# Kernel optimization log

Hardware: AMD Instinct MI355X
Metric: run time of the kernel (lower is better)

Reference implementation:

```python
import math
import jax, jax.numpy as jnp
import numpy as np

B, N, F, FE = 16, 24, 128, 128   # crystals, atoms/crystal, atom feat, edge feat
NUM_Z = 100                       # num_atomic_numbers
GAUSS_STOP, BASIS_W = 6.0, 1.0
RADIUS_RATE = 1.0
N_CONV, N_FC, FC_F = 3, 4, 128
REP = 1                           # PBC replication per axis (27 images); exact for our cells
ZDIM = 2 * F + FE


def setup_inputs() -> dict:
    key = jax.random.key(0)
    ks = jax.random.split(key, 12)
    # cubic cells with side length in [8, 10) Angstrom -> rep per axis is exactly 1
    L = 8.0 + 2.0 * jax.random.uniform(ks[0], (B,))
    cell = L[:, None, None] * jnp.eye(3, dtype=jnp.float32)          # [B,3,3]
    frac = jax.random.uniform(ks[1], (B, N, 3))
    pos = jnp.einsum('bnd,bde->bne', frac, cell).reshape(B * N, 3)   # [B*N,3]
    atomic_numbers = jax.random.randint(ks[2], (B * N,), 1, NUM_Z + 1)
    batch = jnp.repeat(jnp.arange(B), N)
    emb = jax.random.normal(ks[3], (NUM_Z, F)) * 0.1                 # embedding table
    s = 1.0 / math.sqrt(ZDIM)
    conv_Wf = jax.random.normal(ks[4], (N_CONV, ZDIM, F)) * s
    conv_bf = jnp.zeros((N_CONV, F))
    conv_Ws = jax.random.normal(ks[5], (N_CONV, ZDIM, F)) * s
    conv_bs = jnp.zeros((N_CONV, F))
    sf = 1.0 / math.sqrt(FC_F)
    fc_W = jax.random.normal(ks[6], (N_FC - 1, FC_F, FC_F)) * sf
    fc_b = jnp.zeros((N_FC - 1, FC_F))
    W_out = jax.random.normal(ks[7], (FC_F, 1)) * sf
    b_out = jnp.zeros((1,))
    return {'pos': pos, 'cell': cell, 'emb': emb,
            'conv_Wf': conv_Wf, 'conv_bf': conv_bf,
            'conv_Ws': conv_Ws, 'conv_bs': conv_bs,
            'fc_W': fc_W, 'fc_b': fc_b, 'W_out': W_out, 'b_out': b_out,
            'atomic_numbers': atomic_numbers, 'batch': batch}


def _spectral_normalize(W, iters=5, eps=1e-12):
    # power iteration; sigma differentiable through W only (u,v detached) as in torch
    u = jnp.ones((W.shape[1],), W.dtype)
    u = u / jnp.linalg.norm(u)
    for _ in range(iters):
        v = W @ u
        v = v / (jnp.linalg.norm(v) + eps)
        u = W.T @ v
        u = u / (jnp.linalg.norm(u) + eps)
    u = jax.lax.stop_gradient(u)
    v = jax.lax.stop_gradient(v)
    sigma = v @ (W @ u)
    return W / sigma


def _forward(pos, cell, emb, conv_Wf, conv_bf, conv_Ws, conv_bs,
             fc_W, fc_b, W_out, b_out, atomic_numbers):
    # ---- graph construction (PBC all-pairs, fixed 27 images, masked) ----
    r = jnp.arange(-REP, REP + 1, dtype=cell.dtype)
    grid = jnp.stack(jnp.meshgrid(r, r, r, indexing='ij'), -1).reshape(-1, 3)  # [27,3]
    pbc = jnp.einsum('cd,bde->bce', grid, cell)                                # [B,27,3]
    posb = pos.reshape(B, N, 3)
    # disp[b,i,j,c] = pos_i - (pos_j + offset_c)
    disp = posb[:, :, None, None, :] - (posb[:, None, :, None, :] + pbc[:, None, None, :, :])
    dsqr = jnp.sum(disp * disp, -1)                                            # [B,N,N,27]
    cross = jnp.cross(cell[:, 1], cell[:, 2])
    vol = jnp.sum(cell[:, 0] * cross, -1)
    radius = RADIUS_RATE * (jnp.abs(vol) / N) ** (1.0 / 3.0)                   # [B]
    rb = radius[:, None, None, None]
    mask = (dsqr <= rb * rb) & (dsqr > 1e-4)
    dist = jnp.sqrt(jnp.maximum(dsqr, 1e-12))
    mf = mask.astype(pos.dtype)
    edge_w = (jnp.cos(dist * math.pi / rb) + 1.0) * mf                         # [B,N,N,27]
    # GaussianSmearing
    goff = jnp.linspace(0.0, GAUSS_STOP, FE)
    coeff = -0.5 / (BASIS_W * (goff[1] - goff[0])) ** 2
    edge_attr = jnp.exp(coeff * (dist[..., None] - goff) ** 2)                 # [B,N,N,27,FE]

    # ---- node features ----
    feat = jnp.tanh(emb[atomic_numbers - 1]).reshape(B, N, F)

    # ---- continuous graph convs (CGCNN-style gated conv, edge_weight scaled) ----
    for l in range(N_CONV):
        Wf, Ws = conv_Wf[l], conv_Ws[l]
        gi = feat @ Wf[:F]; gj = feat @ Wf[F:2 * F]
        ge = jnp.einsum('bijce,ef->bijcf', edge_attr, Wf[2 * F:])
        g = jax.nn.sigmoid(gi[:, :, None, None, :] + gj[:, None, :, None, :] + ge + conv_bf[l])
        si = feat @ Ws[:F]; sj = feat @ Ws[F:2 * F]
        se = jnp.einsum('bijce,ef->bijcf', edge_attr, Ws[2 * F:])
        sc = jax.nn.softplus(si[:, :, None, None, :] + sj[:, None, :, None, :] + se + conv_bs[l])
        msg = g * sc * edge_w[..., None]                                       # [B,N,N,27,F]
        feat = jax.nn.softplus(feat + msg.sum((2, 3)))                         # aggregate at i

    # ---- global mean pool + spectral-norm MLP head ----
    h = feat.mean(1)                                                           # [B,F]
    for l in range(N_FC - 1):
        h = jax.nn.softplus(h @ _spectral_normalize(fc_W[l]) + fc_b[l])
    return h @ W_out + b_out                                                   # [B,1]


def reference(pos, cell, emb, conv_Wf, conv_bf, conv_Ws, conv_bs,
              fc_W, fc_b, W_out, b_out, atomic_numbers, batch):
    return _forward(pos, cell, emb, conv_Wf, conv_bf, conv_Ws, conv_bs,
                    fc_W, fc_b, W_out, b_out, atomic_numbers)
```

## Files before the change

kernel.cpp:

```cpp
#include <hip/hip_runtime.h>
#include <math.h>

#define NB 16
#define NN 24
#define NA 384
#define FF 128
#define CC 27
#define MAXNBR 32

__device__ int   g_cnt[NA];
__device__ float g_sigma[4];
__device__ int   g_nj[NA*MAXNBR];
__device__ float g_nd[NA*MAXNBR];
__device__ float g_nw[NA*MAXNBR];
__device__ float g_featA[NA*FF];
__device__ float g_featB[NA*FF];
__device__ float g_projA[NA*4*FF];
__device__ float g_projB[NA*4*FF];
__device__ float g_feat [NA*FF];
__device__ int   g_arrF[NB];

__device__ __forceinline__ float softplusf(float x){ return fmaxf(x,0.f) + log1pf(expf(-fabsf(x))); }
__device__ __forceinline__ float sigmoidf(float x){ return 1.f/(1.f+expf(-x)); }
__device__ __forceinline__ void st_agent(float* p, float v){
  __hip_atomic_store(p, v, __ATOMIC_RELAXED, __HIP_MEMORY_SCOPE_AGENT);
}
__device__ __forceinline__ float ld_agent(const float* p){
  return __hip_atomic_load(p, __ATOMIC_RELAXED, __HIP_MEMORY_SCOPE_AGENT);
}

__device__ __forceinline__ void band_dot(float dist, const float* __restrict__ Wf2,
                                         const float* __restrict__ Ws2, int f,
                                         float& ge, float& se)
{
  const float step  = 6.0f/127.0f;
  const float coeff = -0.5f/(step*step);
  int kmin = (int)ceilf(dist/step - 9.0f);
  kmin = kmin < 0 ? 0 : (kmin > 108 ? 108 : kmin);
  float g = 0.f, s = 0.f;
  #pragma unroll
  for (int t = 0; t < 20; t++) {
    int k = kmin + t;
    float dd = dist - step*(float)k;
    float a  = expf(coeff*dd*dd);
    g += a * Wf2[k*FF+f];
    s += a * Ws2[k*FF+f];
  }
  ge = g; se = s;
}

__global__ void __launch_bounds__(512)
k_prep(const float* __restrict__ pos, const float* __restrict__ cell,
       const float* __restrict__ emb, const float* __restrict__ fc_W,
       const float* __restrict__ conv_Wf, const float* __restrict__ conv_Ws,
       const int* __restrict__ z)
{
  const int bid = blockIdx.x, tid = threadIdx.x;
  const int q = tid >> 7, f = tid & 127;

  if (bid < 3) {
    __shared__ float s_w[FF*129];
    __shared__ float s_u[FF], s_v[FF], s_red[FF];
    __shared__ float s_part[4][FF];
    const float* W = fc_W + bid*FF*FF;
    for (int idx = tid; idx < FF*FF; idx += 512)
      s_w[(idx >> 7)*129 + (idx & 127)] = W[idx];
    if (tid < FF) s_u[tid] = 0.08838834764831845f;
    __syncthreads();
    for (int it = 0; it < 5; it++) {
      { float p = 0.f;
        #pragma unroll
        for (int k = q*32; k < q*32+32; k++) p += s_w[f*129+k]*s_u[k];
        s_part[q][f] = p; }
      __syncthreads();
      if (tid < FF) { float s = s_part[0][f]+s_part[1][f]+s_part[2][f]+s_part[3][f];
                      s_v[f] = s; s_red[f] = s*s; }
      __syncthreads();
      for (int st=64; st>0; st>>=1){ if (tid<st) s_red[tid]+=s_red[tid+st]; __syncthreads(); }
      float nv = sqrtf(s_red[0]) + 1e-12f;
      __syncthreads();
      if (tid < FF) s_v[f] /= nv;
      __syncthreads();
      { float p = 0.f;
        #pragma unroll
        for (int r = q*32; r < q*32+32; r++) p += s_w[r*129+f]*s_v[r];
        s_part[q][f] = p; }
      __syncthreads();
      if (tid < FF) { float s = s_part[0][f]+s_part[1][f]+s_part[2][f]+s_part[3][f];
                      s_u[f] = s; s_red[f] = s*s; }
      __syncthreads();
      for (int st=64; st>0; st>>=1){ if (tid<st) s_red[tid]+=s_red[tid+st]; __syncthreads(); }
      float nu = sqrtf(s_red[0]) + 1e-12f;
      __syncthreads();
      if (tid < FF) s_u[f] /= nu;
      __syncthreads();
    }
    { float p = 0.f;
      #pragma unroll
      for (int k = q*32; k < q*32+32; k++) p += s_w[f*129+k]*s_u[k];
      s_part[q][f] = p; }
    __syncthreads();
    if (tid < FF) s_red[f] = s_v[f]*(s_part[0][f]+s_part[1][f]+s_part[2][f]+s_part[3][f]);
    __syncthreads();
    for (int st=64; st>0; st>>=1){ if (tid<st) s_red[tid]+=s_red[tid+st]; __syncthreads(); }
    if (tid == 0) g_sigma[bid] = s_red[0];
  } else {
    const int i = bid - 3;
    const int b = i / NN;
    __shared__ float ft[FF];
    __shared__ float s_cell[9];
    __shared__ float s_rb;
    __shared__ int   s_cnt;
    if (tid < FF) {
      int zi = z[i]; if (zi < 1) zi = 1; if (zi > 100) zi = 100;
      float v = tanhf(emb[(zi-1)*FF+tid]);
      ft[tid] = v;
      g_featA[i*FF+tid] = v;
    }
    if (tid >= 256 && tid < 265) s_cell[tid-256] = cell[b*9 + tid - 256];
    if (tid == 500) s_cnt = 0;
    __syncthreads();
    if (tid == 0) {
      const float* c = s_cell;
      float cx = c[4]*c[8] - c[5]*c[7];
      float cy = c[5]*c[6] - c[3]*c[8];
      float cz = c[3]*c[7] - c[4]*c[6];
      float vol = c[0]*cx + c[1]*cy + c[2]*cz;
      s_rb = cbrtf(fabsf(vol)/(float)NN);
    }
    __syncthreads();
    const float rb = s_rb, rb2 = rb*rb;
    const float pix = pos[i*3+0], piy = pos[i*3+1], piz = pos[i*3+2];
    const float PI = 3.14159265358979323846f;
    for (int cand = tid; cand < NN*CC; cand += 512) {
      int j = cand / CC, c = cand - j*CC;
      float gx = (float)(c/9) - 1.0f;
      float gy = (float)((c/3)%3) - 1.0f;
      float gz = (float)(c%3) - 1.0f;
      float ox = gx*s_cell[0] + gy*s_cell[3] + gz*s_cell[6];
      float oy = gx*s_cell[1] + gy*s_cell[4] + gz*s_cell[7];
      float oz = gx*s_cell[2] + gy*s_cell[5] + gz*s_cell[8];
      int jg = b*NN + j;
      float dx = pix - (pos[jg*3+0] + ox);
      float dy = piy - (pos[jg*3+1] + oy);
      float dz = piz - (pos[jg*3+2] + oz);
      float d2 = dx*dx + dy*dy + dz*dz;
      if (d2 <= rb2 && d2 > 1e-4f) {
        float dist = sqrtf(fmaxf(d2, 1e-12f));
        float w = cosf(dist*PI/rb) + 1.0f;
        int slot = atomicAdd(&s_cnt, 1);
        if (slot < MAXNBR) {
          g_nj[i*MAXNBR+slot] = jg;
          g_nd[i*MAXNBR+slot] = dist;
          g_nw[i*MAXNBR+slot] = w;
        }
      }
    }
    __syncthreads();
    if (tid == 0) g_cnt[i] = (s_cnt > MAXNBR) ? MAXNBR : s_cnt;
    const float* W = (q==0) ? conv_Wf
                   : (q==1) ? (conv_Wf + FF*FF)
                   : (q==2) ? conv_Ws
                   :          (conv_Ws + FF*FF);
    float s = 0.f;
    #pragma unroll 16
    for (int k=0;k<FF;k++) s += ft[k]*W[k*FF+f];
    g_projA[(i*4+q)*FF+f] = s;
  }
}

template<int LAYER>
__global__ void __launch_bounds__(512)
k_edge(const float* __restrict__ conv_Wf, const float* __restrict__ conv_bf,
       const float* __restrict__ conv_Ws, const float* __restrict__ conv_bs)
{
  const int i = blockIdx.x, tid = threadIdx.x;
  const int q = tid >> 7, f = tid & 127;
  const float* projSrc = (LAYER==0) ? g_projA : g_projB;
  float*       projDst = (LAYER==0) ? g_projB : g_projA;
  const float* fin  = (LAYER==0) ? g_featA : g_featB;
  float*       fout = (LAYER==0) ? g_featB : g_featA;
  const float* Wf2 = conv_Wf + LAYER*3*FF*FF + 2*FF*FF;
  const float* Ws2 = conv_Ws + LAYER*3*FF*FF + 2*FF*FF;

  const float gi  = projSrc[(i*4+0)*FF+f];
  const float si  = projSrc[(i*4+2)*FF+f];
  const float bff = conv_bf[LAYER*FF+f];
  const float bsf = conv_bs[LAYER*FF+f];
  const int n = g_cnt[i];

  float msg = 0.f;
  for (int e = q; e < n; e += 4) {
    const int   jg   = g_nj[i*MAXNBR+e];
    const float dist = g_nd[i*MAXNBR+e];
    const float w    = g_nw[i*MAXNBR+e];
    const float gj   = projSrc[(jg*4+1)*FF+f];
    const float sj   = projSrc[(jg*4+3)*FF+f];
    float ge, se;
    band_dot(dist, Wf2, Ws2, f, ge, se);
    msg += sigmoidf(gi + gj + ge + bff) * softplusf(si + sj + se + bsf) * w;
  }

  __shared__ float sm[4][FF];
  __shared__ float fnew[FF];
  sm[q][f] = msg;
  __syncthreads();
  if (tid < FF) {
    float v = softplusf(fin[i*FF+f] + sm[0][f] + sm[1][f] + sm[2][f] + sm[3][f]);
    fnew[f] = v;
    fout[i*FF+f] = v;
  }
  __syncthreads();
  const float* WfN = conv_Wf + (LAYER+1)*3*FF*FF;
  const float* WsN = conv_Ws + (LAYER+1)*3*FF*FF;
  const float* W = (q==0) ? WfN : (q==1) ? (WfN + FF*FF) : (q==2) ? WsN : (WsN + FF*FF);
  float s = 0.f;
  #pragma unroll 16
  for (int k=0;k<FF;k++) s += fnew[k]*W[k*FF+f];
  projDst[(i*4+q)*FF+f] = s;
}

__global__ void __launch_bounds__(512)
k_edge2f(const float* __restrict__ conv_Wf, const float* __restrict__ conv_bf,
         const float* __restrict__ conv_Ws, const float* __restrict__ conv_bs,
         const float* __restrict__ fc_W,  const float* __restrict__ fc_b,
         const float* __restrict__ W_out, const float* __restrict__ b_out,
         float* __restrict__ out)
{
  const int i = blockIdx.x, tid = threadIdx.x;
  const int q = tid >> 7, f = tid & 127;
  const int b = i / NN;
  const float* Wf2 = conv_Wf + 2*3*FF*FF + 2*FF*FF;
  const float* Ws2 = conv_Ws + 2*3*FF*FF + 2*FF*FF;

  const float gi  = g_projA[(i*4+0)*FF+f];
  const float si  = g_projA[(i*4+2)*FF+f];
  const float bff = conv_bf[2*FF+f];
  const float bsf = conv_bs[2*FF+f];
  const int n = g_cnt[i];

  float msg = 0.f;
  for (int e = q; e < n; e += 4) {
    const int   jg   = g_nj[i*MAXNBR+e];
    const float dist = g_nd[i*MAXNBR+e];
    const float w    = g_nw[i*MAXNBR+e];
    const float gj   = g_projA[(jg*4+1)*FF+f];
    const float sj   = g_projA[(jg*4+3)*FF+f];
    float ge, se;
    band_dot(dist, Wf2, Ws2, f, ge, se);
    msg += sigmoidf(gi + gj + ge + bff) * softplusf(si + sj + se + bsf) * w;
  }

  __shared__ float sm[4][FF];
  __shared__ int   s_old;
  sm[q][f] = msg;
  __syncthreads();
  if (tid < FF) {
    float v = softplusf(g_featA[i*FF+f] + sm[0][f] + sm[1][f] + sm[2][f] + sm[3][f]);
    st_agent(&g_feat[i*FF+f], v);
  }
  asm volatile("s_waitcnt vmcnt(0)" ::: "memory");
  __syncthreads();
  if (tid == 0)
    s_old = __hip_atomic_fetch_add(&g_arrF[b], 1, __ATOMIC_ACQ_REL,
                                   __HIP_MEMORY_SCOPE_AGENT);
  __syncthreads();
  if (s_old != NN-1) return;

  __shared__ float s_hh[FF], s_tmp[FF], s_part[4][FF], s_red[FF];
  if (tid < FF) {
    float s0 = 0.f;
    for (int a = 0; a < NN; a++) s0 += ld_agent(&g_feat[(b*NN+a)*FF+tid]);
    s_hh[tid] = s0/(float)NN;
  }
  __syncthreads();
  for (int l = 0; l < 3; l++) {
    { float p = 0.f;
      #pragma unroll
      for (int k = q*32; k < q*32+32; k++) p += s_hh[k]*fc_W[l*FF*FF + k*FF + f];
      s_part[q][f] = p; }
    __syncthreads();
    if (tid < FF) {
      float s = s_part[0][tid]+s_part[1][tid]+s_part[2][tid]+s_part[3][tid];
      s_tmp[tid] = softplusf(s/g_sigma[l] + fc_b[l*FF+tid]);
    }
    __syncthreads();
    if (tid < FF) s_hh[tid] = s_tmp[tid];
    __syncthreads();
  }
  if (tid < FF) s_red[tid] = s_hh[tid]*W_out[tid];
  __syncthreads();
  if (tid < 64) {
    float t = s_red[tid] + s_red[tid+64];
    #pragma unroll
    for (int off = 32; off > 0; off >>= 1) t += __shfl_xor(t, off);
    if (tid == 0) {
      out[b] = t + b_out[0];
      __hip_atomic_store(&g_arrF[b], 0, __ATOMIC_RELAXED,
                         __HIP_MEMORY_SCOPE_AGENT);
    }
  }
}

extern "C" void kernel_launch(void* const* d_in, const int* in_sizes, int n_in,
                              void* d_out, int out_size, void* d_ws, size_t ws_size,
                              hipStream_t stream) {
  const float* pos     = (const float*)d_in[0];
  const float* cell    = (const float*)d_in[1];
  const float* emb     = (const float*)d_in[2];
  const float* conv_Wf = (const float*)d_in[3];
  const float* conv_bf = (const float*)d_in[4];
  const float* conv_Ws = (const float*)d_in[5];
  const float* conv_bs = (const float*)d_in[6];
  const float* fc_W    = (const float*)d_in[7];
  const float* fc_b    = (const float*)d_in[8];
  const float* W_out   = (const float*)d_in[9];
  const float* b_out   = (const float*)d_in[10];
  const int*   z       = (const int*)d_in[11];

  k_prep   <<<NA+3, 512, 0, stream>>>(pos, cell, emb, fc_W, conv_Wf, conv_Ws, z);
  k_edge<0><<<NA,   512, 0, stream>>>(conv_Wf, conv_bf, conv_Ws, conv_bs);
  k_edge<1><<<NA,   512, 0, stream>>>(conv_Wf, conv_bf, conv_Ws, conv_bs);
  k_edge2f <<<NA,   512, 0, stream>>>(conv_Wf, conv_bf, conv_Ws, conv_bs,
                                      fc_W, fc_b, W_out, b_out, (float*)d_out);
}
```

Measured before the change: 138.5 us.

## Fuse all stages into one persistent kernel with per-crystal spin barriers

Replaces the four kernel launches with a single fused kernel. Each atom block keeps its neighbor list, features and projections in shared memory, and blocks of the same crystal synchronize through global atomic counters instead of kernel boundaries. This removes launch gaps and global round-trips for neighbor lists and features, and the spectral-norm blocks now read weights straight from global memory rather than staging them in LDS. It relies on all 387 blocks being co-resident, otherwise the spin-waits can deadlock or hit the guard and compute wrong results.

```diff
diff --git a/kernel.cpp b/kernel.cpp
--- a/kernel.cpp
+++ b/kernel.cpp
@@ -8,17 +8,13 @@
 #define CC 27
 #define MAXNBR 32
 
-__device__ int   g_cnt[NA];
 __device__ float g_sigma[4];
-__device__ int   g_nj[NA*MAXNBR];
-__device__ float g_nd[NA*MAXNBR];
-__device__ float g_nw[NA*MAXNBR];
-__device__ float g_featA[NA*FF];
-__device__ float g_featB[NA*FF];
 __device__ float g_projA[NA*4*FF];
 __device__ float g_projB[NA*4*FF];
 __device__ float g_feat [NA*FF];
-__device__ int   g_arrF[NB];
+__device__ int   g_cnt4 [4*NB];
+__device__ int   g_sigdone;
+__device__ int   g_batchdone;
 
 __device__ __forceinline__ float softplusf(float x){ return fmaxf(x,0.f) + log1pf(expf(-fabsf(x))); }
 __device__ __forceinline__ float sigmoidf(float x){ return 1.f/(1.f+expf(-x)); }
@@ -49,86 +45,165 @@
   ge = g; se = s;
 }
 
-__global__ void __launch_bounds__(512)
-k_prep(const float* __restrict__ pos, const float* __restrict__ cell,
-       const float* __restrict__ emb, const float* __restrict__ fc_W,
-       const float* __restrict__ conv_Wf, const float* __restrict__ conv_Ws,
-       const int* __restrict__ z)
-{
-  const int bid = blockIdx.x, tid = threadIdx.x;
+__device__ __forceinline__ float gemv_q(const float* __restrict__ Wf,
+                                        const float* __restrict__ Ws,
+                                        const float* s_ft, int q, int f)
+{
+  const float* W = (q==0) ? Wf : (q==1) ? (Wf + FF*FF) : (q==2) ? Ws : (Ws + FF*FF);
+  float s = 0.f;
+  #pragma unroll 16
+  for (int k = 0; k < FF; k++) s += s_ft[k]*W[k*FF+f];
+  return s;
+}
+
+__device__ __forceinline__ void publish(int* ctr)
+{
+  asm volatile("s_waitcnt vmcnt(0)" ::: "memory");
+  __syncthreads();
+  if (threadIdx.x == 0)
+    __hip_atomic_fetch_add(ctr, 1, __ATOMIC_RELEASE, __HIP_MEMORY_SCOPE_AGENT);
+}
+
+__device__ __forceinline__ void wait_ge(int* ctr, int target)
+{
+  if (threadIdx.x == 0) {
+    int guard = 0;
+    while (__hip_atomic_load(ctr, __ATOMIC_ACQUIRE, __HIP_MEMORY_SCOPE_AGENT) < target) {
+      __builtin_amdgcn_s_sleep(2);
+      if (++guard > (1<<20)) break;
+    }
+  }
+  __syncthreads();
+}
+
+__device__ __forceinline__ void edge_layer(int l, int q, int f, int n, int i,
+       const float* __restrict__ projSrc,
+       const float* __restrict__ conv_Wf, const float* __restrict__ conv_bf,
+       const float* __restrict__ conv_Ws, const float* __restrict__ conv_bs,
+       const int* s_nj, const float* s_nd, const float* s_nw,
+       float (*s_p)[FF], float (*sm)[FF], float* s_ft)
+{
+  const float* Wf2 = conv_Wf + l*3*FF*FF + 2*FF*FF;
+  const float* Ws2 = conv_Ws + l*3*FF*FF + 2*FF*FF;
+  const float gi  = s_p[0][f];
+  const float si  = s_p[2][f];
+  const float bff = conv_bf[l*FF+f];
+  const float bsf = conv_bs[l*FF+f];
+  float msg = 0.f;
+  for (int e = q; e < n; e += 4) {
+    const int   jg   = s_nj[e];
+    const float dist = s_nd[e];
+    const float w    = s_nw[e];
+    const float gj   = ld_agent(&projSrc[(jg*4+1)*FF+f]);
+    const float sj   = ld_agent(&projSrc[(jg*4+3)*FF+f]);
+    float ge, se;
+    band_dot(dist, Wf2, Ws2, f, ge, se);
+    msg += sigmoidf(gi + gj + ge + bff) * softplusf(si + sj + se + bsf) * w;
+  }
+  sm[q][f] = msg;
+  __syncthreads();
+  if (threadIdx.x < FF) {
+    float v = softplusf(s_ft[f] + sm[0][f] + sm[1][f] + sm[2][f] + sm[3][f]);
+    s_ft[f] = v;
+  }
+  __syncthreads();
+}
+
+__global__ void __launch_bounds__(512, 4)
+k_fused(const float* __restrict__ pos, const float* __restrict__ cell,
+        const float* __restrict__ emb,
+        const float* __restrict__ conv_Wf, const float* __restrict__ conv_bf,
+        const float* __restrict__ conv_Ws, const float* __restrict__ conv_bs,
+        const float* __restrict__ fc_W,  const float* __restrict__ fc_b,
+        const float* __restrict__ W_out, const float* __restrict__ b_out,
+        const int* __restrict__ z, float* __restrict__ out)
+{
+  const int tid = threadIdx.x;
   const int q = tid >> 7, f = tid & 127;
 
-  if (bid < 3) {
-    __shared__ float s_w[FF*129];
-    __shared__ float s_u[FF], s_v[FF], s_red[FF];
-    __shared__ float s_part[4][FF];
-    const float* W = fc_W + bid*FF*FF;
-    for (int idx = tid; idx < FF*FF; idx += 512)
-      s_w[(idx >> 7)*129 + (idx & 127)] = W[idx];
+  if (blockIdx.x < 3) {
+    const int m = blockIdx.x;
+    const float* W = fc_W + m*FF*FF;
+    __shared__ float s_u[FF], s_v[FF], s_red2[FF];
+    __shared__ float s_part2[4][FF];
     if (tid < FF) s_u[tid] = 0.08838834764831845f;
     __syncthreads();
     for (int it = 0; it < 5; it++) {
       { float p = 0.f;
         #pragma unroll
-        for (int k = q*32; k < q*32+32; k++) p += s_w[f*129+k]*s_u[k];
-        s_part[q][f] = p; }
-      __syncthreads();
-      if (tid < FF) { float s = s_part[0][f]+s_part[1][f]+s_part[2][f]+s_part[3][f];
-                      s_v[f] = s; s_red[f] = s*s; }
-      __syncthreads();
-      for (int st=64; st>0; st>>=1){ if (tid<st) s_red[tid]+=s_red[tid+st]; __syncthreads(); }
-      float nv = sqrtf(s_red[0]) + 1e-12f;
+        for (int k = q*32; k < q*32+32; k++) p += W[f*FF+k]*s_u[k];
+        s_part2[q][f] = p; }
+      __syncthreads();
+      if (tid < FF) { float s = s_part2[0][f]+s_part2[1][f]+s_part2[2][f]+s_part2[3][f];
+                      s_v[f] = s; s_red2[f] = s*s; }
+      __syncthreads();
+      for (int st=64; st>0; st>>=1){ if (tid<st) s_red2[tid]+=s_red2[tid+st]; __syncthreads(); }
+      float nv = sqrtf(s_red2[0]) + 1e-12f;
       __syncthreads();
       if (tid < FF) s_v[f] /= nv;
       __syncthreads();
       { float p = 0.f;
         #pragma unroll
-        for (int r = q*32; r < q*32+32; r++) p += s_w[r*129+f]*s_v[r];
-        s_part[q][f] = p; }
-      __syncthreads();
-      if (tid < FF) { float s = s_part[0][f]+s_part[1][f]+s_part[2][f]+s_part[3][f];
-                      s_u[f] = s; s_red[f] = s*s; }
-      __syncthreads();
-      for (int st=64; st>0; st>>=1){ if (tid<st) s_red[tid]+=s_red[tid+st]; __syncthreads(); }
-      float nu = sqrtf(s_red[0]) + 1e-12f;
+        for (int r = q*32; r < q*32+32; r++) p += W[r*FF+f]*s_v[r];
+        s_part2[q][f] = p; }
+      __syncthreads();
+      if (tid < FF) { float s = s_part2[0][f]+s_part2[1][f]+s_part2[2][f]+s_part2[3][f];
+                      s_u[f] = s; s_red2[f] = s*s; }
+      __syncthreads();
+      for (int st=64; st>0; st>>=1){ if (tid<st) s_red2[tid]+=s_red2[tid+st]; __syncthreads(); }
+      float nu = sqrtf(s_red2[0]) + 1e-12f;
       __syncthreads();
       if (tid < FF) s_u[f] /= nu;
       __syncthreads();
     }
     { float p = 0.f;
       #pragma unroll
-      for (int k = q*32; k < q*32+32; k++) p += s_w[f*129+k]*s_u[k];
-      s_part[q][f] = p; }
-    __syncthreads();
-    if (tid < FF) s_red[f] = s_v[f]*(s_part[0][f]+s_part[1][f]+s_part[2][f]+s_part[3][f]);
-    __syncthreads();
-    for (int st=64; st>0; st>>=1){ if (tid<st) s_red[tid]+=s_red[tid+st]; __syncthreads(); }
-    if (tid == 0) g_sigma[bid] = s_red[0];
-  } else {
-    const int i = bid - 3;
-    const int b = i / NN;
-    __shared__ float ft[FF];
-    __shared__ float s_cell[9];
-    __shared__ float s_rb;
-    __shared__ int   s_cnt;
-    if (tid < FF) {
-      int zi = z[i]; if (zi < 1) zi = 1; if (zi > 100) zi = 100;
-      float v = tanhf(emb[(zi-1)*FF+tid]);
-      ft[tid] = v;
-      g_featA[i*FF+tid] = v;
-    }
-    if (tid >= 256 && tid < 265) s_cell[tid-256] = cell[b*9 + tid - 256];
-    if (tid == 500) s_cnt = 0;
-    __syncthreads();
+      for (int k = q*32; k < q*32+32; k++) p += W[f*FF+k]*s_u[k];
+      s_part2[q][f] = p; }
+    __syncthreads();
+    if (tid < FF) s_red2[f] = s_v[f]*(s_part2[0][f]+s_part2[1][f]+s_part2[2][f]+s_part2[3][f]);
+    __syncthreads();
+    for (int st=64; st>0; st>>=1){ if (tid<st) s_red2[tid]+=s_red2[tid+st]; __syncthreads(); }
     if (tid == 0) {
-      const float* c = s_cell;
-      float cx = c[4]*c[8] - c[5]*c[7];
-      float cy = c[5]*c[6] - c[3]*c[8];
-      float cz = c[3]*c[7] - c[4]*c[6];
-      float vol = c[0]*cx + c[1]*cy + c[2]*cz;
-      s_rb = cbrtf(fabsf(vol)/(float)NN);
-    }
-    __syncthreads();
+      st_agent(&g_sigma[m], s_red2[0]);
+      asm volatile("s_waitcnt vmcnt(0)" ::: "memory");
+      __hip_atomic_fetch_add(&g_sigdone, 1, __ATOMIC_RELEASE, __HIP_MEMORY_SCOPE_AGENT);
+    }
+    return;
+  }
+
+  const int i = (int)blockIdx.x - 3;
+  const int b = i / NN;
+
+  __shared__ float s_ft[FF];
+  __shared__ float s_cell[9];
+  __shared__ float s_rb;
+  __shared__ int   s_cnt;
+  __shared__ int   s_nj[MAXNBR];
+  __shared__ float s_nd[MAXNBR];
+  __shared__ float s_nw[MAXNBR];
+  __shared__ float s_p[4][FF];
+  __shared__ float sm[4][FF];
+  __shared__ int   s_last;
+  __shared__ float s_hh[FF], s_tmp[FF], s_red[FF];
+
+  if (tid < FF) {
+    int zi = z[i]; if (zi < 1) zi = 1; if (zi > 100) zi = 100;
+    s_ft[tid] = tanhf(emb[(zi-1)*FF+tid]);
+  }
+  if (tid >= 256 && tid < 265) s_cell[tid-256] = cell[b*9 + tid - 256];
+  if (tid == 500) s_cnt = 0;
+  __syncthreads();
+  if (tid == 0) {
+    const float* c = s_cell;
+    float cx = c[4]*c[8] - c[5]*c[7];
+    float cy = c[5]*c[6] - c[3]*c[8];
+    float cz = c[3]*c[7] - c[4]*c[6];
+    float vol = c[0]*cx + c[1]*cy + c[2]*cz;
+    s_rb = cbrtf(fabsf(vol)/(float)NN);
+  }
+  __syncthreads();
+  {
     const float rb = s_rb, rb2 = rb*rb;
     const float pix = pos[i*3+0], piy = pos[i*3+1], piz = pos[i*3+2];
     const float PI = 3.14159265358979323846f;
@@ -149,125 +224,54 @@
         float dist = sqrtf(fmaxf(d2, 1e-12f));
         float w = cosf(dist*PI/rb) + 1.0f;
         int slot = atomicAdd(&s_cnt, 1);
-        if (slot < MAXNBR) {
-          g_nj[i*MAXNBR+slot] = jg;
-          g_nd[i*MAXNBR+slot] = dist;
-          g_nw[i*MAXNBR+slot] = w;
-        }
+        if (slot < MAXNBR) { s_nj[slot] = jg; s_nd[slot] = dist; s_nw[slot] = w; }
       }
     }
-    __syncthreads();
-    if (tid == 0) g_cnt[i] = (s_cnt > MAXNBR) ? MAXNBR : s_cnt;
-    const float* W = (q==0) ? conv_Wf
-                   : (q==1) ? (conv_Wf + FF*FF)
-                   : (q==2) ? conv_Ws
-                   :          (conv_Ws + FF*FF);
-    float s = 0.f;
-    #pragma unroll 16
-    for (int k=0;k<FF;k++) s += ft[k]*W[k*FF+f];
-    g_projA[(i*4+q)*FF+f] = s;
-  }
-}
-
-template<int LAYER>
-__global__ void __launch_bounds__(512)
-k_edge(const float* __restrict__ conv_Wf, const float* __restrict__ conv_bf,
-       const float* __restrict__ conv_Ws, const float* __restrict__ conv_bs)
-{
-  const int i = blockIdx.x, tid = threadIdx.x;
-  const int q = tid >> 7, f = tid & 127;
-  const float* projSrc = (LAYER==0) ? g_projA : g_projB;
-  float*       projDst = (LAYER==0) ? g_projB : g_projA;
-  const float* fin  = (LAYER==0) ? g_featA : g_featB;
-  float*       fout = (LAYER==0) ? g_featB : g_featA;
-  const float* Wf2 = conv_Wf + LAYER*3*FF*FF + 2*FF*FF;
-  const float* Ws2 = conv_Ws + LAYER*3*FF*FF + 2*FF*FF;
-
-  const float gi  = projSrc[(i*4+0)*FF+f];
-  const float si  = projSrc[(i*4+2)*FF+f];
-  const float bff = conv_bf[LAYER*FF+f];
-  const float bsf = conv_bs[LAYER*FF+f];
-  const int n = g_cnt[i];
-
-  float msg = 0.f;
-  for (int e = q; e < n; e += 4) {
-    const int   jg   = g_nj[i*MAXNBR+e];
-    const float dist = g_nd[i*MAXNBR+e];
-    const float w    = g_nw[i*MAXNBR+e];
-    const float gj   = projSrc[(jg*4+1)*FF+f];
-    const float sj   = projSrc[(jg*4+3)*FF+f];
-    float ge, se;
-    band_dot(dist, Wf2, Ws2, f, ge, se);
-    msg += sigmoidf(gi + gj + ge + bff) * softplusf(si + sj + se + bsf) * w;
-  }
-
-  __shared__ float sm[4][FF];
-  __shared__ float fnew[FF];
-  sm[q][f] = msg;
-  __syncthreads();
-  if (tid < FF) {
-    float v = softplusf(fin[i*FF+f] + sm[0][f] + sm[1][f] + sm[2][f] + sm[3][f]);
-    fnew[f] = v;
-    fout[i*FF+f] = v;
-  }
-  __syncthreads();
-  const float* WfN = conv_Wf + (LAYER+1)*3*FF*FF;
-  const float* WsN = conv_Ws + (LAYER+1)*3*FF*FF;
-  const float* W = (q==0) ? WfN : (q==1) ? (WfN + FF*FF) : (q==2) ? WsN : (WsN + FF*FF);
-  float s = 0.f;
-  #pragma unroll 16
-  for (int k=0;k<FF;k++) s += fnew[k]*W[k*FF+f];
-  projDst[(i*4+q)*FF+f] = s;
-}
-
-__global__ void __launch_bounds__(512)
-k_edge2f(const float* __restrict__ conv_Wf, const float* __restrict__ conv_bf,
-         const float* __restrict__ conv_Ws, const float* __restrict__ conv_bs,
-         const float* __restrict__ fc_W,  const float* __restrict__ fc_b,
-         const float* __restrict__ W_out, const float* __restrict__ b_out,
-         float* __restrict__ out)
-{
-  const int i = blockIdx.x, tid = threadIdx.x;
-  const int q = tid >> 7, f = tid & 127;
-  const int b = i / NN;
-  const float* Wf2 = conv_Wf + 2*3*FF*FF + 2*FF*FF;
-  const float* Ws2 = conv_Ws + 2*3*FF*FF + 2*FF*FF;
-
-  const float gi  = g_projA[(i*4+0)*FF+f];
-  const float si  = g_projA[(i*4+2)*FF+f];
-  const float bff = conv_bf[2*FF+f];
-  const float bsf = conv_bs[2*FF+f];
-  const int n = g_cnt[i];
-
-  float msg = 0.f;
-  for (int e = q; e < n; e += 4) {
-    const int   jg   = g_nj[i*MAXNBR+e];
-    const float dist = g_nd[i*MAXNBR+e];
-    const float w    = g_nw[i*MAXNBR+e];
-    const float gj   = g_projA[(jg*4+1)*FF+f];
-    const float sj   = g_projA[(jg*4+3)*FF+f];
-    float ge, se;
-    band_dot(dist, Wf2, Ws2, f, ge, se);
-    msg += sigmoidf(gi + gj + ge + bff) * softplusf(si + sj + se + bsf) * w;
-  }
-
-  __shared__ float sm[4][FF];
-  __shared__ int   s_old;
-  sm[q][f] = msg;
-  __syncthreads();
-  if (tid < FF) {
-    float v = softplusf(g_featA[i*FF+f] + sm[0][f] + sm[1][f] + sm[2][f] + sm[3][f]);
-    st_agent(&g_feat[i*FF+f], v);
-  }
+  }
+  __syncthreads();
+  const int n = (s_cnt > MAXNBR) ? MAXNBR : s_cnt;
+
+  { float s0 = gemv_q(conv_Wf, conv_Ws, s_ft, q, f);
+    s_p[q][f] = s0;
+    st_agent(&g_projA[(i*4+q)*FF+f], s0); }
+  publish(&g_cnt4[0*NB+b]);
+  wait_ge(&g_cnt4[0*NB+b], NN);
+
+  edge_layer(0, q, f, n, i, g_projA, conv_Wf, conv_bf, conv_Ws, conv_bs,
+             s_nj, s_nd, s_nw, s_p, sm, s_ft);
+  { float s1 = gemv_q(conv_Wf + 3*FF*FF, conv_Ws + 3*FF*FF, s_ft, q, f);
+    s_p[q][f] = s1;
+    st_agent(&g_projB[(i*4+q)*FF+f], s1); }
+  publish(&g_cnt4[1*NB+b]);
+  wait_ge(&g_cnt4[1*NB+b], NN);
+
+  edge_layer(1, q, f, n, i, g_projB, conv_Wf, conv_bf, conv_Ws, conv_bs,
+             s_nj, s_nd, s_nw, s_p, sm, s_ft);
+  { float s2 = gemv_q(conv_Wf + 2*3*FF*FF, conv_Ws + 2*3*FF*FF, s_ft, q, f);
+    s_p[q][f] = s2;
+    st_agent(&g_projA[(i*4+q)*FF+f], s2); }
+  publish(&g_cnt4[2*NB+b]);
+  wait_ge(&g_cnt4[2*NB+b], NN);
+
+  edge_layer(2, q, f, n, i, g_projA, conv_Wf, conv_bf, conv_Ws, conv_bs,
+             s_nj, s_nd, s_nw, s_p, sm, s_ft);
+  if (tid < FF) st_agent(&g_feat[i*FF+f], s_ft[f]);
   asm volatile("s_waitcnt vmcnt(0)" ::: "memory");
   __syncthreads();
   if (tid == 0)
-    s_old = __hip_atomic_fetch_add(&g_arrF[b], 1, __ATOMIC_ACQ_REL,
-                                   __HIP_MEMORY_SCOPE_AGENT);
-  __syncthreads();
-  if (s_old != NN-1) return;
-
-  __shared__ float s_hh[FF], s_tmp[FF], s_part[4][FF], s_red[FF];
+    s_last = __hip_atomic_fetch_add(&g_cnt4[3*NB+b], 1, __ATOMIC_ACQ_REL,
+                                    __HIP_MEMORY_SCOPE_AGENT);
+  __syncthreads();
+  if (s_last != NN-1) return;
+
+  if (tid == 0) {
+    int guard = 0;
+    while (__hip_atomic_load(&g_sigdone, __ATOMIC_ACQUIRE, __HIP_MEMORY_SCOPE_AGENT) < 3) {
+      __builtin_amdgcn_s_sleep(2);
+      if (++guard > (1<<20)) break;
+    }
+  }
+  __syncthreads();
   if (tid < FF) {
     float s0 = 0.f;
     for (int a = 0; a < NN; a++) s0 += ld_agent(&g_feat[(b*NN+a)*FF+tid]);
@@ -278,11 +282,11 @@
     { float p = 0.f;
       #pragma unroll
       for (int k = q*32; k < q*32+32; k++) p += s_hh[k]*fc_W[l*FF*FF + k*FF + f];
-      s_part[q][f] = p; }
+      sm[q][f] = p; }
     __syncthreads();
     if (tid < FF) {
-      float s = s_part[0][tid]+s_part[1][tid]+s_part[2][tid]+s_part[3][tid];
-      s_tmp[tid] = softplusf(s/g_sigma[l] + fc_b[l*FF+tid]);
+      float s = sm[0][tid]+sm[1][tid]+sm[2][tid]+sm[3][tid];
+      s_tmp[tid] = softplusf(s/ld_agent(&g_sigma[l]) + fc_b[l*FF+tid]);
     }
     __syncthreads();
     if (tid < FF) s_hh[tid] = s_tmp[tid];
@@ -296,8 +300,16 @@
     for (int off = 32; off > 0; off >>= 1) t += __shfl_xor(t, off);
     if (tid == 0) {
       out[b] = t + b_out[0];
-      __hip_atomic_store(&g_arrF[b], 0, __ATOMIC_RELAXED,
-                         __HIP_MEMORY_SCOPE_AGENT);
+      __hip_atomic_store(&g_cnt4[0*NB+b], 0, __ATOMIC_RELAXED, __HIP_MEMORY_SCOPE_AGENT);
+      __hip_atomic_store(&g_cnt4[1*NB+b], 0, __ATOMIC_RELAXED, __HIP_MEMORY_SCOPE_AGENT);
+      __hip_atomic_store(&g_cnt4[2*NB+b], 0, __ATOMIC_RELAXED, __HIP_MEMORY_SCOPE_AGENT);
+      __hip_atomic_store(&g_cnt4[3*NB+b], 0, __ATOMIC_RELAXED, __HIP_MEMORY_SCOPE_AGENT);
+      int d = __hip_atomic_fetch_add(&g_batchdone, 1, __ATOMIC_ACQ_REL,
+                                     __HIP_MEMORY_SCOPE_AGENT);
+      if (d == NB-1) {
+        __hip_atomic_store(&g_batchdone, 0, __ATOMIC_RELAXED, __HIP_MEMORY_SCOPE_AGENT);
+        __hip_atomic_store(&g_sigdone,   0, __ATOMIC_RELAXED, __HIP_MEMORY_SCOPE_AGENT);
+      }
     }
   }
 }
@@ -318,9 +330,7 @@
   const float* b_out   = (const float*)d_in[10];
   const int*   z       = (const int*)d_in[11];
 
-  k_prep   <<<NA+3, 512, 0, stream>>>(pos, cell, emb, fc_W, conv_Wf, conv_Ws, z);
-  k_edge<0><<<NA,   512, 0, stream>>>(conv_Wf, conv_bf, conv_Ws, conv_bs);
-  k_edge<1><<<NA,   512, 0, stream>>>(conv_Wf, conv_bf, conv_Ws, conv_bs);
-  k_edge2f <<<NA,   512, 0, stream>>>(conv_Wf, conv_bf, conv_Ws, conv_bs,
-                                      fc_W, fc_b, W_out, b_out, (float*)d_out);
-}
+  k_fused<<<NA+3, 512, 0, stream>>>(pos, cell, emb, conv_Wf, conv_bf,
+                                    conv_Ws, conv_bs, fc_W, fc_b,
+                                    W_out, b_out, z, (float*)d_out);
+}
```

New measurement: 273.8 us. +97.8%, slower.
